# Performance work log

Hardware: AMD Instinct MI355X
Metric: run time of the kernel (lower is better)

Reference implementation:

```python
import jax, jax.numpy as jnp
import numpy as np

A, L, D_ATOM, D_PROT, B = 2048, 512, 128, 128, 64
H1, H2 = 512, 256


def setup_inputs() -> dict:
    key = jax.random.key(0)
    ks = jax.random.split(key, 10)
    atom_embed = jax.random.normal(ks[0], (A, D_ATOM), dtype=jnp.float32)
    protSeq_embed = jax.random.normal(ks[1], (B, L, D_PROT), dtype=jnp.float32)
    atom_splits = jnp.sort(jax.random.randint(ks[2], (A,), 0, B))
    # attention bilinear weight (atom_dim, prot_dim); scaled so exp(score) stays finite
    W_att = jax.random.normal(ks[3], (D_ATOM, D_PROT), dtype=jnp.float32) / np.float32(D_ATOM)
    cdim = D_ATOM + D_PROT
    W1 = jax.random.normal(ks[4], (cdim, H1), dtype=jnp.float32) / np.sqrt(np.float32(cdim))
    b1 = jnp.zeros((H1,), dtype=jnp.float32)
    W2 = jax.random.normal(ks[5], (H1, H2), dtype=jnp.float32) / np.sqrt(np.float32(H1))
    b2 = jnp.zeros((H2,), dtype=jnp.float32)
    Wo = jax.random.normal(ks[6], (H2, 1), dtype=jnp.float32) / np.sqrt(np.float32(H2))
    bo = jnp.zeros((1,), dtype=jnp.float32)
    return {"atom_embed": atom_embed, "protSeq_embed": protSeq_embed,
            "atom_splits": atom_splits, "W_att": W_att,
            "W1": W1, "b1": b1, "W2": W2, "b2": b2, "Wo": Wo, "bo": bo}


def reference(atom_embed, protSeq_embed, atom_splits, W_att, W1, b1, W2, b2, Wo, bo):
    batch = protSeq_embed.shape[0]
    # bilinear attention scores: S[a, l] = atom[a] @ W_att @ prot[seg[a], l]
    X = atom_embed @ W_att                              # [A, D_PROT]
    prot_g = protSeq_embed[atom_splits]                 # [A, L, D_PROT] (gather)
    S = jnp.einsum('ad,ald->al', X, prot_g)             # [A, L]
    # segment softmax over atoms within each molecule (on max-over-protein score)
    Wc = jnp.exp(jnp.max(S, axis=-1, keepdims=True))    # [A, 1]
    Sc = jax.ops.segment_sum(Wc, atom_splits, num_segments=batch)[atom_splits]
    aa = Wc / Sc                                        # [A, 1]
    atom_pool = jax.ops.segment_sum(aa * atom_embed, atom_splits, num_segments=batch)  # [B, D_ATOM]
    # protein attention: segment-max pooled scores -> softmax over residues
    Wp = jax.ops.segment_max(S, atom_splits, num_segments=batch)  # [B, L]
    ap = jax.nn.softmax(Wp, axis=-1)
    prot_pool = jnp.einsum('bl,bld->bd', ap, protSeq_embed)       # [B, D_PROT]
    h = jnp.concatenate([atom_pool, prot_pool], axis=-1)
    h = jax.nn.relu(h @ W1 + b1)
    h = jax.nn.relu(h @ W2 + b2)
    return h @ Wo + bo                                  # [B, 1]
```

## Files before the change

kernel.cpp:

```cpp
#include <hip/hip_runtime.h>
#include <math.h>

#define A_N 2048
#define L_N 512
#define D 128
#define B_N 64
#define H1_N 512
#define H2_N 256
#define NCHUNK 16
#define CL 32

typedef __attribute__((ext_vector_type(8))) short short8;
typedef __attribute__((ext_vector_type(4))) float f32x4;

__device__ __forceinline__ int lb_dev(const int* __restrict__ arr, int n, int val) {
    int lo = 0, hi = n;
    while (lo < hi) { int mid = (lo + hi) >> 1; if (arr[mid] < val) lo = mid + 1; else hi = mid; }
    return lo;
}

__device__ __forceinline__ float blk_sum(float v, float* red, int tid) {
    #pragma unroll
    for (int off = 32; off >= 1; off >>= 1) v += __shfl_xor(v, off);
    __syncthreads();
    if ((tid & 63) == 0) red[tid >> 6] = v;
    __syncthreads();
    return red[0] + red[1] + red[2] + red[3];
}

__device__ __forceinline__ unsigned short f2bf(float f) {
    unsigned int u = __float_as_uint(f);
    return (unsigned short)((u + 0x7FFFu + ((u >> 16) & 1u)) >> 16);
}
__device__ __forceinline__ float bf2f(unsigned short h) {
    return __uint_as_float(((unsigned int)h) << 16);
}

__global__ __launch_bounds__(256) void k1_xmul(const float* __restrict__ atom_embed,
                                               const float* __restrict__ W_att,
                                               const float* __restrict__ bo,
                                               const int* __restrict__ splits,
                                               unsigned short* __restrict__ Xh,
                                               unsigned short* __restrict__ Xl,
                                               float* __restrict__ out,
                                               int* __restrict__ segoff) {
    __shared__ float ae[8][128];
    const int tid = threadIdx.x;
    const int bid = blockIdx.x;
    if (bid == 0) {
        if (tid < B_N) out[tid] = bo[0];
        if (tid <= B_N) segoff[tid] = lb_dev(splits, A_N, tid);
    }
    const int a0 = bid * 8;
    float4 v = reinterpret_cast<const float4*>(atom_embed + (size_t)a0 * D)[tid];
    const int fi = tid * 4;
    *reinterpret_cast<float4*>(&ae[fi >> 7][fi & 127]) = v;
    __syncthreads();
    const int d = tid & 127;
    const int ai = tid >> 7;
    float acc0 = 0.f, acc1 = 0.f, acc2 = 0.f, acc3 = 0.f;
    #pragma unroll 16
    for (int k = 0; k < D; ++k) {
        const float w = W_att[k * D + d];
        acc0 += ae[ai + 0][k] * w;
        acc1 += ae[ai + 2][k] * w;
        acc2 += ae[ai + 4][k] * w;
        acc3 += ae[ai + 6][k] * w;
    }
    float accs[4] = {acc0, acc1, acc2, acc3};
    #pragma unroll
    for (int t = 0; t < 4; ++t) {
        const size_t idx = (size_t)(a0 + ai + 2 * t) * D + d;
        const unsigned short h = f2bf(accs[t]);
        Xh[idx] = h;
        Xl[idx] = f2bf(accs[t] - bf2f(h));
    }
}

__global__ __launch_bounds__(256, 3) void k2_scores(const unsigned short* __restrict__ Xh,
                                                    const unsigned short* __restrict__ Xl,
                                                    const float* __restrict__ prot,
                                                    const int* __restrict__ segoff,
                                                    float* __restrict__ rowmaxp,
                                                    float* __restrict__ ppart,
                                                    float* __restrict__ eWpart) {
    __shared__ float rm_part[2][128];
    __shared__ float cm_part[2][32];
    __shared__ float ews_s[CL];
    __shared__ float4 pred[8][32];

    const int tid = threadIdx.x;
    const int bid = blockIdx.x;
    const int b = bid & (B_N - 1);
    const int chunk = bid >> 6;
    const int l0 = chunk * CL;

    const int lane = tid & 63;
    const int w = tid >> 6;
    const int col = lane & 15;
    const int kb = lane >> 4;
    const int lt = w & 1;
    const int pair = w >> 1;

    short8 Bh[4], Bl[4];
    {
        const float4* pb = (const float4*)(prot + ((size_t)(b * L_N + l0 + lt * 16 + col)) * D);
        #pragma unroll
        for (int ks = 0; ks < 4; ++ks) {
            const float4 v0 = pb[ks * 8 + kb * 2];
            const float4 v1 = pb[ks * 8 + kb * 2 + 1];
            const float vv[8] = {v0.x, v0.y, v0.z, v0.w, v1.x, v1.y, v1.z, v1.w};
            short8 bh, bl;
            #pragma unroll
            for (int j = 0; j < 8; ++j) {
                const unsigned short h = f2bf(vv[j]);
                bh[j] = (short)h;
                bl[j] = (short)f2bf(vv[j] - bf2f(h));
            }
            Bh[ks] = bh; Bl[ks] = bl;
        }
    }
    const int s = segoff[b];
    const int n = segoff[b + 1] - s;

    ((float*)rm_part)[tid] = -INFINITY;
    if (tid < 64) ((float*)cm_part)[tid] = -INFINITY;
    __syncthreads();

    float cmrun = -INFINITY;
    for (int at = pair; at * 16 < n; at += 2) {
        const int arow = min(s + at * 16 + col, A_N - 1);
        const unsigned short* xh = Xh + (size_t)arow * D;
        const unsigned short* xl = Xl + (size_t)arow * D;
        short8 Ah[4], Al[4];
        #pragma unroll
        for (int ks = 0; ks < 4; ++ks) {
            Ah[ks] = *(const short8*)(xh + ks * 32 + kb * 8);
            Al[ks] = *(const short8*)(xl + ks * 32 + kb * 8);
        }
        f32x4 aHH = {0.f, 0.f, 0.f, 0.f};
        f32x4 aHL = {0.f, 0.f, 0.f, 0.f};
        f32x4 aLH = {0.f, 0.f, 0.f, 0.f};
        #pragma unroll
        for (int ks = 0; ks < 4; ++ks) {
            aHH = __builtin_amdgcn_mfma_f32_16x16x32_bf16(Ah[ks], Bh[ks], aHH, 0, 0, 0);
            aHL = __builtin_amdgcn_mfma_f32_16x16x32_bf16(Ah[ks], Bl[ks], aHL, 0, 0, 0);
            aLH = __builtin_amdgcn_mfma_f32_16x16x32_bf16(Al[ks], Bh[ks], aLH, 0, 0, 0);
        }
        float r[4];
        #pragma unroll
        for (int i = 0; i < 4; ++i) r[i] = aHH[i] + aHL[i] + aLH[i];

        float r0 = r[0], r1 = r[1], r2 = r[2], r3 = r[3];
        #pragma unroll
        for (int off = 1; off <= 8; off <<= 1) {
            r0 = fmaxf(r0, __shfl_xor(r0, off));
            r1 = fmaxf(r1, __shfl_xor(r1, off));
            r2 = fmaxf(r2, __shfl_xor(r2, off));
            r3 = fmaxf(r3, __shfl_xor(r3, off));
        }
        if (col == 0) {
            rm_part[lt][at * 16 + kb * 4 + 0] = r0;
            rm_part[lt][at * 16 + kb * 4 + 1] = r1;
            rm_part[lt][at * 16 + kb * 4 + 2] = r2;
            rm_part[lt][at * 16 + kb * 4 + 3] = r3;
        }
        const int rb = at * 16 + kb * 4;
        float cm = -INFINITY;
        if (rb + 0 < n) cm = fmaxf(cm, r[0]);
        if (rb + 1 < n) cm = fmaxf(cm, r[1]);
        if (rb + 2 < n) cm = fmaxf(cm, r[2]);
        if (rb + 3 < n) cm = fmaxf(cm, r[3]);
        cm = fmaxf(cm, __shfl_xor(cm, 16));
        cm = fmaxf(cm, __shfl_xor(cm, 32));
        cmrun = fmaxf(cmrun, cm);
    }
    if (kb == 0) cm_part[pair][lt * 16 + col] = cmrun;
    __syncthreads();

    if (tid < 128 && tid < n)
        rowmaxp[(size_t)(s + tid) * NCHUNK + chunk] = fmaxf(rm_part[0][tid], rm_part[1][tid]);
    if (tid >= 128 && tid < 128 + CL) {
        const int l = tid - 128;
        ews_s[l] = expf(fmaxf(cm_part[0][l], cm_part[1][l]));
    }
    __syncthreads();

    if (tid < 32) {
        float v = ews_s[tid];
        #pragma unroll
        for (int off = 1; off <= 16; off <<= 1) v += __shfl_xor(v, off);
        if (tid == 0) eWpart[b * NCHUNK + chunk] = v;
    }

    const int rg = tid >> 5, c4 = tid & 31;
    float4 pp4 = {0.f, 0.f, 0.f, 0.f};
    const float4* src = (const float4*)(prot + ((size_t)b * L_N + l0) * D);
    #pragma unroll
    for (int q = 0; q < 4; ++q) {
        const int i = tid + q * 256;
        const float4 v = src[i];
        const float wgt = ews_s[i >> 5];
        pp4.x += wgt * v.x; pp4.y += wgt * v.y;
        pp4.z += wgt * v.z; pp4.w += wgt * v.w;
    }
    pred[rg][c4] = pp4;
    __syncthreads();
    if (tid < 32) {
        float4 acc = pred[0][tid];
        #pragma unroll
        for (int gg = 1; gg < 8; ++gg) {
            const float4 t = pred[gg][tid];
            acc.x += t.x; acc.y += t.y; acc.z += t.z; acc.w += t.w;
        }
        float* dst = ppart + (size_t)(b * NCHUNK + chunk) * D + tid * 4;
        dst[0] = acc.x; dst[1] = acc.y; dst[2] = acc.z; dst[3] = acc.w;
    }
}

__global__ __launch_bounds__(256) void k3_pool(const float* __restrict__ atom_embed,
                                               const int* __restrict__ segoff,
                                               const float* __restrict__ rowmaxp,
                                               const float* __restrict__ ppart,
                                               const float* __restrict__ eWpart,
                                               float* __restrict__ HcT) {
    __shared__ float red[4];
    __shared__ float coef[512];
    __shared__ float4 pred[8][32];
    const int tid = threadIdx.x;
    const int b = blockIdx.x;
    const int s = segoff[b];
    const int n = segoff[b + 1] - s;

    float local = 0.f;
    for (int j = tid; j < n; j += 256) {
        const float* rp = rowmaxp + (size_t)(s + j) * NCHUNK;
        float m = rp[0];
        #pragma unroll
        for (int c = 1; c < NCHUNK; ++c) m = fmaxf(m, rp[c]);
        local += expf(m);
    }
    const float Sc = blk_sum(local, red, tid);

    const int d4 = tid & 31;
    const int ag = tid >> 5;
    const float4* ae4 = reinterpret_cast<const float4*>(atom_embed);
    float4 pool = {0.f, 0.f, 0.f, 0.f};
    for (int t0 = 0; t0 < n; t0 += 512) {
        const int cnt = min(512, n - t0);
        __syncthreads();
        for (int j = tid; j < cnt; j += 256) {
            const float* rp = rowmaxp + (size_t)(s + t0 + j) * NCHUNK;
            float m = rp[0];
            #pragma unroll
            for (int c = 1; c < NCHUNK; ++c) m = fmaxf(m, rp[c]);
            coef[j] = expf(m) / Sc;
        }
        __syncthreads();
        #pragma unroll 4
        for (int j = ag; j < cnt; j += 8) {
            const float c = coef[j];
            const float4 v = ae4[(size_t)(s + t0 + j) * (D / 4) + d4];
            pool.x += c * v.x; pool.y += c * v.y; pool.z += c * v.z; pool.w += c * v.w;
        }
    }
    __syncthreads();
    pred[ag][d4] = pool;
    __syncthreads();
    if (ag == 0) {
        float4 acc = pred[0][d4];
        #pragma unroll
        for (int gg = 1; gg < 8; ++gg) {
            const float4 t = pred[gg][d4];
            acc.x += t.x; acc.y += t.y; acc.z += t.z; acc.w += t.w;
        }
        HcT[(size_t)(d4 * 4 + 0) * B_N + b] = acc.x;
        HcT[(size_t)(d4 * 4 + 1) * B_N + b] = acc.y;
        HcT[(size_t)(d4 * 4 + 2) * B_N + b] = acc.z;
        HcT[(size_t)(d4 * 4 + 3) * B_N + b] = acc.w;
    }
    if (tid < 128) {
        float v = 0.f, ez = 0.f;
        #pragma unroll
        for (int c = 0; c < NCHUNK; ++c) {
            v  += ppart[(size_t)(b * NCHUNK + c) * D + tid];
            ez += eWpart[b * NCHUNK + c];
        }
        HcT[(size_t)(D + tid) * B_N + b] = v / ez;
    }
}

__global__ __launch_bounds__(256) void k4_h1(const float* __restrict__ HcT,
                                             const float* __restrict__ W1,
                                             const float* __restrict__ b1,
                                             float* __restrict__ H1T) {
    __shared__ float hr[4][64];
    const int tid = threadIdx.x;
    const int m = tid & 63;
    const int jh = (tid >> 6) & 1;
    const int kh = tid >> 7;
    const int j = blockIdx.x * 2 + jh;
    float acc = 0.f;
    const int k0 = kh * 128;
    #pragma unroll 8
    for (int k = k0; k < k0 + 128; ++k)
        acc += HcT[(size_t)k * B_N + m] * W1[(size_t)k * H1_N + j];
    hr[jh * 2 + kh][m] = acc;
    __syncthreads();
    if (kh == 0)
        H1T[(size_t)j * B_N + m] = fmaxf(hr[jh * 2][m] + hr[jh * 2 + 1][m] + b1[j], 0.f);
}

__global__ __launch_bounds__(256) void k5_h2(const float* __restrict__ H1T,
                                             const float* __restrict__ W2,
                                             const float* __restrict__ b2,
                                             const float* __restrict__ Wo,
                                             float* __restrict__ out) {
    __shared__ float hr[4][64];
    const int tid = threadIdx.x;
    const int m = tid & 63;
    const int kq = tid >> 6;
    const int j = blockIdx.x;
    float acc = 0.f;
    const int k0 = kq * 128;
    #pragma unroll 8
    for (int k = k0; k < k0 + 128; ++k)
        acc += H1T[(size_t)k * B_N + m] * W2[(size_t)k * H2_N + j];
    hr[kq][m] = acc;
    __syncthreads();
    if (kq == 0) {
        const float h2 = fmaxf(hr[0][m] + hr[1][m] + hr[2][m] + hr[3][m] + b2[j], 0.f);
        atomicAdd(out + m, h2 * Wo[j]);
    }
}

extern "C" void kernel_launch(void* const* d_in, const int* in_sizes, int n_in,
                              void* d_out, int out_size, void* d_ws, size_t ws_size,
                              hipStream_t stream) {
    const float* atom_embed = (const float*)d_in[0];
    const float* prot       = (const float*)d_in[1];
    const int*   splits     = (const int*)d_in[2];
    const float* W_att      = (const float*)d_in[3];
    const float* W1         = (const float*)d_in[4];
    const float* b1         = (const float*)d_in[5];
    const float* W2         = (const float*)d_in[6];
    const float* b2         = (const float*)d_in[7];
    const float* Wo         = (const float*)d_in[8];
    const float* bo         = (const float*)d_in[9];
    float* out = (float*)d_out;

    unsigned short* Xh = (unsigned short*)d_ws;
    unsigned short* Xl = Xh + (size_t)A_N * D;
    float* fp      = (float*)(Xl + (size_t)A_N * D);
    float* rowmaxp = fp;  fp += (size_t)A_N * NCHUNK;
    float* ppart   = fp;  fp += (size_t)B_N * NCHUNK * D;
    float* eWpart  = fp;  fp += B_N * NCHUNK;
    float* HcT     = fp;  fp += 2 * D * B_N;
    float* H1T     = fp;  fp += H1_N * B_N;
    int*   segoff  = (int*)fp;

    hipLaunchKernelGGL(k1_xmul,  dim3(A_N / 8),        dim3(256), 0, stream,
                       atom_embed, W_att, bo, splits, Xh, Xl, out, segoff);
    hipLaunchKernelGGL(k2_scores, dim3(B_N * NCHUNK),  dim3(256), 0, stream,
                       Xh, Xl, prot, segoff, rowmaxp, ppart, eWpart);
    hipLaunchKernelGGL(k3_pool,  dim3(B_N),            dim3(256), 0, stream,
                       atom_embed, segoff, rowmaxp, ppart, eWpart, HcT);
    hipLaunchKernelGGL(k4_h1,    dim3(H1_N / 2),       dim3(256), 0, stream, HcT, W1, b1, H1T);
    hipLaunchKernelGGL(k5_h2,    dim3(H2_N),           dim3(256), 0, stream, H1T, W2, b2, Wo, out);
}
```

Baseline: 48.40 us.

## Fuse X projection and pooling into scores kernel with last-block reduction

Removes the separate X = atom@W_att kernel and the pooling kernel. Each score block now recomputes X for its molecule's atoms with split-bf16 MFMA into shared memory, then computes scores. The last-arriving chunk block per molecule, found through an atomic counter, does the segment pooling. This cuts two launches and the Xh/Xl round trip through global memory, at the cost of computing X 16 times per atom, reloading and converting W_att in every atom tile, and adding a serial tail in the last block.

```diff
diff --git a/kernel.cpp b/kernel.cpp
--- a/kernel.cpp
+++ b/kernel.cpp
@@ -9,6 +9,7 @@
 #define H2_N 256
 #define NCHUNK 16
 #define CL 32
+#define PST 136
 
 typedef __attribute__((ext_vector_type(8))) short short8;
 typedef __attribute__((ext_vector_type(4))) float f32x4;
@@ -36,58 +37,33 @@
     return __uint_as_float(((unsigned int)h) << 16);
 }
 
-__global__ __launch_bounds__(256) void k1_xmul(const float* __restrict__ atom_embed,
-                                               const float* __restrict__ W_att,
+__global__ __launch_bounds__(256) void k0_init(const int* __restrict__ splits,
                                                const float* __restrict__ bo,
-                                               const int* __restrict__ splits,
-                                               unsigned short* __restrict__ Xh,
-                                               unsigned short* __restrict__ Xl,
-                                               float* __restrict__ out,
-                                               int* __restrict__ segoff) {
-    __shared__ float ae[8][128];
+                                               int* __restrict__ segoff,
+                                               int* __restrict__ cnt,
+                                               float* __restrict__ out) {
     const int tid = threadIdx.x;
-    const int bid = blockIdx.x;
-    if (bid == 0) {
-        if (tid < B_N) out[tid] = bo[0];
-        if (tid <= B_N) segoff[tid] = lb_dev(splits, A_N, tid);
-    }
-    const int a0 = bid * 8;
-    float4 v = reinterpret_cast<const float4*>(atom_embed + (size_t)a0 * D)[tid];
-    const int fi = tid * 4;
-    *reinterpret_cast<float4*>(&ae[fi >> 7][fi & 127]) = v;
-    __syncthreads();
-    const int d = tid & 127;
-    const int ai = tid >> 7;
-    float acc0 = 0.f, acc1 = 0.f, acc2 = 0.f, acc3 = 0.f;
-    #pragma unroll 16
-    for (int k = 0; k < D; ++k) {
-        const float w = W_att[k * D + d];
-        acc0 += ae[ai + 0][k] * w;
-        acc1 += ae[ai + 2][k] * w;
-        acc2 += ae[ai + 4][k] * w;
-        acc3 += ae[ai + 6][k] * w;
-    }
-    float accs[4] = {acc0, acc1, acc2, acc3};
-    #pragma unroll
-    for (int t = 0; t < 4; ++t) {
-        const size_t idx = (size_t)(a0 + ai + 2 * t) * D + d;
-        const unsigned short h = f2bf(accs[t]);
-        Xh[idx] = h;
-        Xl[idx] = f2bf(accs[t] - bf2f(h));
-    }
-}
-
-__global__ __launch_bounds__(256, 3) void k2_scores(const unsigned short* __restrict__ Xh,
-                                                    const unsigned short* __restrict__ Xl,
-                                                    const float* __restrict__ prot,
-                                                    const int* __restrict__ segoff,
-                                                    float* __restrict__ rowmaxp,
-                                                    float* __restrict__ ppart,
-                                                    float* __restrict__ eWpart) {
-    __shared__ float rm_part[2][128];
+    if (tid <= B_N) segoff[tid] = lb_dev(splits, A_N, tid);
+    if (tid < B_N) { cnt[tid] = 0; out[tid] = bo[0]; }
+}
+
+__global__ __launch_bounds__(256, 2) void k2_fused(const float* __restrict__ atom_embed,
+                                                   const float* __restrict__ prot,
+                                                   const float* __restrict__ W_att,
+                                                   const int* __restrict__ segoff,
+                                                   float* __restrict__ rowmaxp,
+                                                   float* __restrict__ ppart,
+                                                   float* __restrict__ eWpart,
+                                                   float* __restrict__ HcT,
+                                                   int* __restrict__ cnt) {
+    __shared__ unsigned short Xs_h[32 * PST], Xs_l[32 * PST];
+    __shared__ float rm_part[2][32];
     __shared__ float cm_part[2][32];
     __shared__ float ews_s[CL];
     __shared__ float4 pred[8][32];
+    __shared__ float coef[256];
+    __shared__ float red[4];
+    __shared__ int isLast;
 
     const int tid = threadIdx.x;
     const int bid = blockIdx.x;
@@ -102,7 +78,7 @@
     const int lt = w & 1;
     const int pair = w >> 1;
 
-    short8 Bh[4], Bl[4];
+    short8 PBh[4], PBl[4];
     {
         const float4* pb = (const float4*)(prot + ((size_t)(b * L_N + l0 + lt * 16 + col)) * D);
         #pragma unroll
@@ -117,94 +93,153 @@
                 bh[j] = (short)h;
                 bl[j] = (short)f2bf(vv[j] - bf2f(h));
             }
-            Bh[ks] = bh; Bl[ks] = bl;
+            PBh[ks] = bh; PBl[ks] = bl;
         }
     }
     const int s = segoff[b];
     const int n = segoff[b + 1] - s;
 
-    ((float*)rm_part)[tid] = -INFINITY;
-    if (tid < 64) ((float*)cm_part)[tid] = -INFINITY;
-    __syncthreads();
-
     float cmrun = -INFINITY;
-    for (int at = pair; at * 16 < n; at += 2) {
-        const int arow = min(s + at * 16 + col, A_N - 1);
-        const unsigned short* xh = Xh + (size_t)arow * D;
-        const unsigned short* xl = Xl + (size_t)arow * D;
-        short8 Ah[4], Al[4];
-        #pragma unroll
-        for (int ks = 0; ks < 4; ++ks) {
-            Ah[ks] = *(const short8*)(xh + ks * 32 + kb * 8);
-            Al[ks] = *(const short8*)(xl + ks * 32 + kb * 8);
-        }
-        f32x4 aHH = {0.f, 0.f, 0.f, 0.f};
-        f32x4 aHL = {0.f, 0.f, 0.f, 0.f};
-        f32x4 aLH = {0.f, 0.f, 0.f, 0.f};
-        #pragma unroll
-        for (int ks = 0; ks < 4; ++ks) {
-            aHH = __builtin_amdgcn_mfma_f32_16x16x32_bf16(Ah[ks], Bh[ks], aHH, 0, 0, 0);
-            aHL = __builtin_amdgcn_mfma_f32_16x16x32_bf16(Ah[ks], Bl[ks], aHL, 0, 0, 0);
-            aLH = __builtin_amdgcn_mfma_f32_16x16x32_bf16(Al[ks], Bh[ks], aLH, 0, 0, 0);
-        }
-        float r[4];
-        #pragma unroll
-        for (int i = 0; i < 4; ++i) r[i] = aHH[i] + aHL[i] + aLH[i];
-
-        float r0 = r[0], r1 = r[1], r2 = r[2], r3 = r[3];
-        #pragma unroll
-        for (int off = 1; off <= 8; off <<= 1) {
-            r0 = fmaxf(r0, __shfl_xor(r0, off));
-            r1 = fmaxf(r1, __shfl_xor(r1, off));
-            r2 = fmaxf(r2, __shfl_xor(r2, off));
-            r3 = fmaxf(r3, __shfl_xor(r3, off));
-        }
-        if (col == 0) {
-            rm_part[lt][at * 16 + kb * 4 + 0] = r0;
-            rm_part[lt][at * 16 + kb * 4 + 1] = r1;
-            rm_part[lt][at * 16 + kb * 4 + 2] = r2;
-            rm_part[lt][at * 16 + kb * 4 + 3] = r3;
-        }
-        const int rb = at * 16 + kb * 4;
-        float cm = -INFINITY;
-        if (rb + 0 < n) cm = fmaxf(cm, r[0]);
-        if (rb + 1 < n) cm = fmaxf(cm, r[1]);
-        if (rb + 2 < n) cm = fmaxf(cm, r[2]);
-        if (rb + 3 < n) cm = fmaxf(cm, r[3]);
-        cm = fmaxf(cm, __shfl_xor(cm, 16));
-        cm = fmaxf(cm, __shfl_xor(cm, 32));
-        cmrun = fmaxf(cmrun, cm);
-    }
+    for (int a0 = 0; a0 < n; a0 += 32) {
+        __syncthreads();
+
+        {
+            short8 WBh[2][4], WBl[2][4];
+            #pragma unroll
+            for (int ct = 0; ct < 2; ++ct) {
+                const int dcol = (w * 2 + ct) * 16 + col;
+                #pragma unroll
+                for (int ks = 0; ks < 4; ++ks) {
+                    short8 bh, bl;
+                    #pragma unroll
+                    for (int j = 0; j < 8; ++j) {
+                        const float wv = W_att[(size_t)(ks * 32 + kb * 8 + j) * D + dcol];
+                        const unsigned short h = f2bf(wv);
+                        bh[j] = (short)h;
+                        bl[j] = (short)f2bf(wv - bf2f(h));
+                    }
+                    WBh[ct][ks] = bh; WBl[ct][ks] = bl;
+                }
+            }
+            #pragma unroll
+            for (int m = 0; m < 2; ++m) {
+                const int ar = min(s + a0 + m * 16 + col, A_N - 1);
+                short8 Ah[4], Al[4];
+                #pragma unroll
+                for (int ks = 0; ks < 4; ++ks) {
+                    const float4* p = (const float4*)(atom_embed + (size_t)ar * D) + ks * 8 + kb * 2;
+                    const float4 v0 = p[0];
+                    const float4 v1 = p[1];
+                    const float vv[8] = {v0.x, v0.y, v0.z, v0.w, v1.x, v1.y, v1.z, v1.w};
+                    short8 ah, al;
+                    #pragma unroll
+                    for (int j = 0; j < 8; ++j) {
+                        const unsigned short h = f2bf(vv[j]);
+                        ah[j] = (short)h;
+                        al[j] = (short)f2bf(vv[j] - bf2f(h));
+                    }
+                    Ah[ks] = ah; Al[ks] = al;
+                }
+                #pragma unroll
+                for (int ct = 0; ct < 2; ++ct) {
+                    f32x4 aHH = {0.f, 0.f, 0.f, 0.f};
+                    f32x4 aHL = {0.f, 0.f, 0.f, 0.f};
+                    f32x4 aLH = {0.f, 0.f, 0.f, 0.f};
+                    #pragma unroll
+                    for (int ks = 0; ks < 4; ++ks) {
+                        aHH = __builtin_amdgcn_mfma_f32_16x16x32_bf16(Ah[ks], WBh[ct][ks], aHH, 0, 0, 0);
+                        aHL = __builtin_amdgcn_mfma_f32_16x16x32_bf16(Ah[ks], WBl[ct][ks], aHL, 0, 0, 0);
+                        aLH = __builtin_amdgcn_mfma_f32_16x16x32_bf16(Al[ks], WBh[ct][ks], aLH, 0, 0, 0);
+                    }
+                    const int dcol = (w * 2 + ct) * 16 + col;
+                    #pragma unroll
+                    for (int i = 0; i < 4; ++i) {
+                        const float xv = aHH[i] + aHL[i] + aLH[i];
+                        const int row = m * 16 + kb * 4 + i;
+                        const unsigned short h = f2bf(xv);
+                        Xs_h[row * PST + dcol] = h;
+                        Xs_l[row * PST + dcol] = f2bf(xv - bf2f(h));
+                    }
+                }
+            }
+        }
+        __syncthreads();
+
+        {
+            short8 Ah[4], Al[4];
+            const int xrow = pair * 16 + col;
+            #pragma unroll
+            for (int ks = 0; ks < 4; ++ks) {
+                Ah[ks] = *(const short8*)(Xs_h + xrow * PST + ks * 32 + kb * 8);
+                Al[ks] = *(const short8*)(Xs_l + xrow * PST + ks * 32 + kb * 8);
+            }
+            f32x4 aHH = {0.f, 0.f, 0.f, 0.f};
+            f32x4 aHL = {0.f, 0.f, 0.f, 0.f};
+            f32x4 aLH = {0.f, 0.f, 0.f, 0.f};
+            #pragma unroll
+            for (int ks = 0; ks < 4; ++ks) {
+                aHH = __builtin_amdgcn_mfma_f32_16x16x32_bf16(Ah[ks], PBh[ks], aHH, 0, 0, 0);
+                aHL = __builtin_amdgcn_mfma_f32_16x16x32_bf16(Ah[ks], PBl[ks], aHL, 0, 0, 0);
+                aLH = __builtin_amdgcn_mfma_f32_16x16x32_bf16(Al[ks], PBh[ks], aLH, 0, 0, 0);
+            }
+            float r[4];
+            #pragma unroll
+            for (int i = 0; i < 4; ++i) r[i] = aHH[i] + aHL[i] + aLH[i];
+
+            float r0 = r[0], r1 = r[1], r2 = r[2], r3 = r[3];
+            #pragma unroll
+            for (int off = 1; off <= 8; off <<= 1) {
+                r0 = fmaxf(r0, __shfl_xor(r0, off));
+                r1 = fmaxf(r1, __shfl_xor(r1, off));
+                r2 = fmaxf(r2, __shfl_xor(r2, off));
+                r3 = fmaxf(r3, __shfl_xor(r3, off));
+            }
+            if (col == 0) {
+                rm_part[lt][pair * 16 + kb * 4 + 0] = r0;
+                rm_part[lt][pair * 16 + kb * 4 + 1] = r1;
+                rm_part[lt][pair * 16 + kb * 4 + 2] = r2;
+                rm_part[lt][pair * 16 + kb * 4 + 3] = r3;
+            }
+            const int rb = a0 + pair * 16 + kb * 4;
+            float cm = -INFINITY;
+            if (rb + 0 < n) cm = fmaxf(cm, r[0]);
+            if (rb + 1 < n) cm = fmaxf(cm, r[1]);
+            if (rb + 2 < n) cm = fmaxf(cm, r[2]);
+            if (rb + 3 < n) cm = fmaxf(cm, r[3]);
+            cm = fmaxf(cm, __shfl_xor(cm, 16));
+            cm = fmaxf(cm, __shfl_xor(cm, 32));
+            cmrun = fmaxf(cmrun, cm);
+        }
+        __syncthreads();
+        if (tid < 32 && a0 + tid < n)
+            rowmaxp[(size_t)(s + a0 + tid) * NCHUNK + chunk] =
+                fmaxf(rm_part[0][tid], rm_part[1][tid]);
+    }
+
     if (kb == 0) cm_part[pair][lt * 16 + col] = cmrun;
     __syncthreads();
-
-    if (tid < 128 && tid < n)
-        rowmaxp[(size_t)(s + tid) * NCHUNK + chunk] = fmaxf(rm_part[0][tid], rm_part[1][tid]);
-    if (tid >= 128 && tid < 128 + CL) {
-        const int l = tid - 128;
-        ews_s[l] = expf(fmaxf(cm_part[0][l], cm_part[1][l]));
-    }
-    __syncthreads();
-
+    if (tid < CL) ews_s[tid] = expf(fmaxf(cm_part[0][tid], cm_part[1][tid]));
+    __syncthreads();
     if (tid < 32) {
         float v = ews_s[tid];
         #pragma unroll
         for (int off = 1; off <= 16; off <<= 1) v += __shfl_xor(v, off);
         if (tid == 0) eWpart[b * NCHUNK + chunk] = v;
     }
-
     const int rg = tid >> 5, c4 = tid & 31;
-    float4 pp4 = {0.f, 0.f, 0.f, 0.f};
-    const float4* src = (const float4*)(prot + ((size_t)b * L_N + l0) * D);
-    #pragma unroll
-    for (int q = 0; q < 4; ++q) {
-        const int i = tid + q * 256;
-        const float4 v = src[i];
-        const float wgt = ews_s[i >> 5];
-        pp4.x += wgt * v.x; pp4.y += wgt * v.y;
-        pp4.z += wgt * v.z; pp4.w += wgt * v.w;
-    }
-    pred[rg][c4] = pp4;
+    {
+        float4 pp4 = {0.f, 0.f, 0.f, 0.f};
+        const float4* src = (const float4*)(prot + ((size_t)b * L_N + l0) * D);
+        #pragma unroll
+        for (int q = 0; q < 4; ++q) {
+            const int i = tid + q * 256;
+            const float4 v = src[i];
+            const float wgt = ews_s[i >> 5];
+            pp4.x += wgt * v.x; pp4.y += wgt * v.y;
+            pp4.z += wgt * v.z; pp4.w += wgt * v.w;
+        }
+        pred[rg][c4] = pp4;
+    }
     __syncthreads();
     if (tid < 32) {
         float4 acc = pred[0][tid];
@@ -216,21 +251,17 @@
         float* dst = ppart + (size_t)(b * NCHUNK + chunk) * D + tid * 4;
         dst[0] = acc.x; dst[1] = acc.y; dst[2] = acc.z; dst[3] = acc.w;
     }
-}
-
-__global__ __launch_bounds__(256) void k3_pool(const float* __restrict__ atom_embed,
-                                               const int* __restrict__ segoff,
-                                               const float* __restrict__ rowmaxp,
-                                               const float* __restrict__ ppart,
-                                               const float* __restrict__ eWpart,
-                                               float* __restrict__ HcT) {
-    __shared__ float red[4];
-    __shared__ float coef[512];
-    __shared__ float4 pred[8][32];
-    const int tid = threadIdx.x;
-    const int b = blockIdx.x;
-    const int s = segoff[b];
-    const int n = segoff[b + 1] - s;
+    __syncthreads();
+
+    if (tid == 0) {
+        __threadfence();
+        int old = __hip_atomic_fetch_add(&cnt[b], 1, __ATOMIC_ACQ_REL, __HIP_MEMORY_SCOPE_AGENT);
+        isLast = (old == NCHUNK - 1) ? 1 : 0;
+    }
+    __syncthreads();
+    if (!isLast) return;
+    if (tid == 0) __threadfence();
+    __syncthreads();
 
     float local = 0.f;
     for (int j = tid; j < n; j += 256) {
@@ -242,14 +273,12 @@
     }
     const float Sc = blk_sum(local, red, tid);
 
-    const int d4 = tid & 31;
-    const int ag = tid >> 5;
-    const float4* ae4 = reinterpret_cast<const float4*>(atom_embed);
+    const float4* ae4 = (const float4*)atom_embed;
     float4 pool = {0.f, 0.f, 0.f, 0.f};
-    for (int t0 = 0; t0 < n; t0 += 512) {
-        const int cnt = min(512, n - t0);
-        __syncthreads();
-        for (int j = tid; j < cnt; j += 256) {
+    for (int t0 = 0; t0 < n; t0 += 256) {
+        const int cnt2 = min(256, n - t0);
+        __syncthreads();
+        for (int j = tid; j < cnt2; j += 256) {
             const float* rp = rowmaxp + (size_t)(s + t0 + j) * NCHUNK;
             float m = rp[0];
             #pragma unroll
@@ -257,27 +286,26 @@
             coef[j] = expf(m) / Sc;
         }
         __syncthreads();
-        #pragma unroll 4
-        for (int j = ag; j < cnt; j += 8) {
+        for (int j = rg; j < cnt2; j += 8) {
             const float c = coef[j];
-            const float4 v = ae4[(size_t)(s + t0 + j) * (D / 4) + d4];
+            const float4 v = ae4[(size_t)(s + t0 + j) * (D / 4) + c4];
             pool.x += c * v.x; pool.y += c * v.y; pool.z += c * v.z; pool.w += c * v.w;
         }
     }
     __syncthreads();
-    pred[ag][d4] = pool;
-    __syncthreads();
-    if (ag == 0) {
-        float4 acc = pred[0][d4];
+    pred[rg][c4] = pool;
+    __syncthreads();
+    if (rg == 0) {
+        float4 acc = pred[0][c4];
         #pragma unroll
         for (int gg = 1; gg < 8; ++gg) {
-            const float4 t = pred[gg][d4];
+            const float4 t = pred[gg][c4];
             acc.x += t.x; acc.y += t.y; acc.z += t.z; acc.w += t.w;
         }
-        HcT[(size_t)(d4 * 4 + 0) * B_N + b] = acc.x;
-        HcT[(size_t)(d4 * 4 + 1) * B_N + b] = acc.y;
-        HcT[(size_t)(d4 * 4 + 2) * B_N + b] = acc.z;
-        HcT[(size_t)(d4 * 4 + 3) * B_N + b] = acc.w;
+        HcT[(size_t)(c4 * 4 + 0) * B_N + b] = acc.x;
+        HcT[(size_t)(c4 * 4 + 1) * B_N + b] = acc.y;
+        HcT[(size_t)(c4 * 4 + 2) * B_N + b] = acc.z;
+        HcT[(size_t)(c4 * 4 + 3) * B_N + b] = acc.w;
     }
     if (tid < 128) {
         float v = 0.f, ez = 0.f;
@@ -349,22 +377,19 @@
     const float* bo         = (const float*)d_in[9];
     float* out = (float*)d_out;
 
-    unsigned short* Xh = (unsigned short*)d_ws;
-    unsigned short* Xl = Xh + (size_t)A_N * D;
-    float* fp      = (float*)(Xl + (size_t)A_N * D);
+    float* fp      = (float*)d_ws;
     float* rowmaxp = fp;  fp += (size_t)A_N * NCHUNK;
     float* ppart   = fp;  fp += (size_t)B_N * NCHUNK * D;
     float* eWpart  = fp;  fp += B_N * NCHUNK;
     float* HcT     = fp;  fp += 2 * D * B_N;
     float* H1T     = fp;  fp += H1_N * B_N;
-    int*   segoff  = (int*)fp;
-
-    hipLaunchKernelGGL(k1_xmul,  dim3(A_N / 8),        dim3(256), 0, stream,
-                       atom_embed, W_att, bo, splits, Xh, Xl, out, segoff);
-    hipLaunchKernelGGL(k2_scores, dim3(B_N * NCHUNK),  dim3(256), 0, stream,
-                       Xh, Xl, prot, segoff, rowmaxp, ppart, eWpart);
-    hipLaunchKernelGGL(k3_pool,  dim3(B_N),            dim3(256), 0, stream,
-                       atom_embed, segoff, rowmaxp, ppart, eWpart, HcT);
-    hipLaunchKernelGGL(k4_h1,    dim3(H1_N / 2),       dim3(256), 0, stream, HcT, W1, b1, H1T);
-    hipLaunchKernelGGL(k5_h2,    dim3(H2_N),           dim3(256), 0, stream, H1T, W2, b2, Wo, out);
-}
+    int*   segoff  = (int*)fp;  fp += 96;
+    int*   cnt     = (int*)fp;  fp += 64;
+
+    hipLaunchKernelGGL(k0_init,  dim3(1),             dim3(256), 0, stream,
+                       splits, bo, segoff, cnt, out);
+    hipLaunchKernelGGL(k2_fused, dim3(B_N * NCHUNK),  dim3(256), 0, stream,
+                       atom_embed, prot, W_att, segoff, rowmaxp, ppart, eWpart, HcT, cnt);
+    hipLaunchKernelGGL(k4_h1,    dim3(H1_N / 2),      dim3(256), 0, stream, HcT, W1, b1, H1T);
+    hipLaunchKernelGGL(k5_h2,    dim3(H2_N),          dim3(256), 0, stream, H1T, W2, b2, Wo, out);
+}
```

New measurement: 90.96 us. +87.9%, slower.

## Rework score and pooling kernels: per-wave 32-residue units, move protein pooling to k3

Applied to the files above, without the earlier changes.

k2 now gives each wave a 32-residue chunk and half the atom tiles, with two B tiles per wave. It writes row maxima straight to global memory and column maxima per half, so the shared-memory reductions and block syncs are gone. The protein-weighted pooling moves from k2 into k3, which now runs on 4x more blocks, each handling a 32-wide slice of the feature dimension. The aim is to shorten k2's critical path and spread k3's work across more CUs. In exchange, the k3 blocks recompute the exp/softmax normalisation redundantly and re-read the protein data.

```diff
diff --git a/kernel.cpp b/kernel.cpp
--- a/kernel.cpp
+++ b/kernel.cpp
@@ -8,7 +8,6 @@
 #define H1_N 512
 #define H2_N 256
 #define NCHUNK 16
-#define CL 32
 
 typedef __attribute__((ext_vector_type(8))) short short8;
 typedef __attribute__((ext_vector_type(4))) float f32x4;
@@ -48,8 +47,8 @@
     const int tid = threadIdx.x;
     const int bid = blockIdx.x;
     if (bid == 0) {
+        if (tid <= B_N) segoff[tid] = lb_dev(splits, A_N, tid);
         if (tid < B_N) out[tid] = bo[0];
-        if (tid <= B_N) segoff[tid] = lb_dev(splits, A_N, tid);
     }
     const int a0 = bid * 8;
     float4 v = reinterpret_cast<const float4*>(atom_embed + (size_t)a0 * D)[tid];
@@ -77,33 +76,26 @@
     }
 }
 
-__global__ __launch_bounds__(256, 3) void k2_scores(const unsigned short* __restrict__ Xh,
-                                                    const unsigned short* __restrict__ Xl,
-                                                    const float* __restrict__ prot,
-                                                    const int* __restrict__ segoff,
-                                                    float* __restrict__ rowmaxp,
-                                                    float* __restrict__ ppart,
-                                                    float* __restrict__ eWpart) {
-    __shared__ float rm_part[2][128];
-    __shared__ float cm_part[2][32];
-    __shared__ float ews_s[CL];
-    __shared__ float4 pred[8][32];
-
+__global__ __launch_bounds__(256) void k2_scores(const unsigned short* __restrict__ Xh,
+                                                 const unsigned short* __restrict__ Xl,
+                                                 const float* __restrict__ prot,
+                                                 const int* __restrict__ segoff,
+                                                 float* __restrict__ rowmaxp,
+                                                 float* __restrict__ cmaxp) {
     const int tid = threadIdx.x;
     const int bid = blockIdx.x;
     const int b = bid & (B_N - 1);
-    const int chunk = bid >> 6;
-    const int l0 = chunk * CL;
-
+    const int unit = (bid >> 6) * 4 + (tid >> 6);
+    const int chunk = unit & 15;
+    const int t0 = unit >> 4;
     const int lane = tid & 63;
-    const int w = tid >> 6;
     const int col = lane & 15;
     const int kb = lane >> 4;
-    const int lt = w & 1;
-    const int pair = w >> 1;
-
-    short8 Bh[4], Bl[4];
-    {
+    const int l0 = chunk * 32;
+
+    short8 Bh[2][4], Bl[2][4];
+    #pragma unroll
+    for (int lt = 0; lt < 2; ++lt) {
         const float4* pb = (const float4*)(prot + ((size_t)(b * L_N + l0 + lt * 16 + col)) * D);
         #pragma unroll
         for (int ks = 0; ks < 4; ++ks) {
@@ -117,19 +109,15 @@
                 bh[j] = (short)h;
                 bl[j] = (short)f2bf(vv[j] - bf2f(h));
             }
-            Bh[ks] = bh; Bl[ks] = bl;
+            Bh[lt][ks] = bh; Bl[lt][ks] = bl;
         }
     }
     const int s = segoff[b];
     const int n = segoff[b + 1] - s;
 
-    ((float*)rm_part)[tid] = -INFINITY;
-    if (tid < 64) ((float*)cm_part)[tid] = -INFINITY;
-    __syncthreads();
-
-    float cmrun = -INFINITY;
-    for (int at = pair; at * 16 < n; at += 2) {
-        const int arow = min(s + at * 16 + col, A_N - 1);
+    float cm0 = -INFINITY, cm1 = -INFINITY;
+    for (int t = t0; t * 16 < n; t += 2) {
+        const int arow = min(s + t * 16 + col, A_N - 1);
         const unsigned short* xh = Xh + (size_t)arow * D;
         const unsigned short* xl = Xl + (size_t)arow * D;
         short8 Ah[4], Al[4];
@@ -138,97 +126,74 @@
             Ah[ks] = *(const short8*)(xh + ks * 32 + kb * 8);
             Al[ks] = *(const short8*)(xl + ks * 32 + kb * 8);
         }
-        f32x4 aHH = {0.f, 0.f, 0.f, 0.f};
-        f32x4 aHL = {0.f, 0.f, 0.f, 0.f};
-        f32x4 aLH = {0.f, 0.f, 0.f, 0.f};
+        f32x4 a0HH = {0.f,0.f,0.f,0.f}, a0HL = {0.f,0.f,0.f,0.f}, a0LH = {0.f,0.f,0.f,0.f};
+        f32x4 a1HH = {0.f,0.f,0.f,0.f}, a1HL = {0.f,0.f,0.f,0.f}, a1LH = {0.f,0.f,0.f,0.f};
         #pragma unroll
         for (int ks = 0; ks < 4; ++ks) {
-            aHH = __builtin_amdgcn_mfma_f32_16x16x32_bf16(Ah[ks], Bh[ks], aHH, 0, 0, 0);
-            aHL = __builtin_amdgcn_mfma_f32_16x16x32_bf16(Ah[ks], Bl[ks], aHL, 0, 0, 0);
-            aLH = __builtin_amdgcn_mfma_f32_16x16x32_bf16(Al[ks], Bh[ks], aLH, 0, 0, 0);
-        }
-        float r[4];
-        #pragma unroll
-        for (int i = 0; i < 4; ++i) r[i] = aHH[i] + aHL[i] + aLH[i];
-
-        float r0 = r[0], r1 = r[1], r2 = r[2], r3 = r[3];
+            a0HH = __builtin_amdgcn_mfma_f32_16x16x32_bf16(Ah[ks], Bh[0][ks], a0HH, 0, 0, 0);
+            a0HL = __builtin_amdgcn_mfma_f32_16x16x32_bf16(Ah[ks], Bl[0][ks], a0HL, 0, 0, 0);
+            a0LH = __builtin_amdgcn_mfma_f32_16x16x32_bf16(Al[ks], Bh[0][ks], a0LH, 0, 0, 0);
+            a1HH = __builtin_amdgcn_mfma_f32_16x16x32_bf16(Ah[ks], Bh[1][ks], a1HH, 0, 0, 0);
+            a1HL = __builtin_amdgcn_mfma_f32_16x16x32_bf16(Ah[ks], Bl[1][ks], a1HL, 0, 0, 0);
+            a1LH = __builtin_amdgcn_mfma_f32_16x16x32_bf16(Al[ks], Bh[1][ks], a1LH, 0, 0, 0);
+        }
+        float ra[4], rb[4];
+        #pragma unroll
+        for (int i = 0; i < 4; ++i) {
+            ra[i] = a0HH[i] + a0HL[i] + a0LH[i];
+            rb[i] = a1HH[i] + a1HL[i] + a1LH[i];
+        }
+        float m0 = fmaxf(ra[0], rb[0]), m1 = fmaxf(ra[1], rb[1]);
+        float m2 = fmaxf(ra[2], rb[2]), m3 = fmaxf(ra[3], rb[3]);
         #pragma unroll
         for (int off = 1; off <= 8; off <<= 1) {
-            r0 = fmaxf(r0, __shfl_xor(r0, off));
-            r1 = fmaxf(r1, __shfl_xor(r1, off));
-            r2 = fmaxf(r2, __shfl_xor(r2, off));
-            r3 = fmaxf(r3, __shfl_xor(r3, off));
+            m0 = fmaxf(m0, __shfl_xor(m0, off));
+            m1 = fmaxf(m1, __shfl_xor(m1, off));
+            m2 = fmaxf(m2, __shfl_xor(m2, off));
+            m3 = fmaxf(m3, __shfl_xor(m3, off));
         }
         if (col == 0) {
-            rm_part[lt][at * 16 + kb * 4 + 0] = r0;
-            rm_part[lt][at * 16 + kb * 4 + 1] = r1;
-            rm_part[lt][at * 16 + kb * 4 + 2] = r2;
-            rm_part[lt][at * 16 + kb * 4 + 3] = r3;
-        }
-        const int rb = at * 16 + kb * 4;
-        float cm = -INFINITY;
-        if (rb + 0 < n) cm = fmaxf(cm, r[0]);
-        if (rb + 1 < n) cm = fmaxf(cm, r[1]);
-        if (rb + 2 < n) cm = fmaxf(cm, r[2]);
-        if (rb + 3 < n) cm = fmaxf(cm, r[3]);
-        cm = fmaxf(cm, __shfl_xor(cm, 16));
-        cm = fmaxf(cm, __shfl_xor(cm, 32));
-        cmrun = fmaxf(cmrun, cm);
-    }
-    if (kb == 0) cm_part[pair][lt * 16 + col] = cmrun;
-    __syncthreads();
-
-    if (tid < 128 && tid < n)
-        rowmaxp[(size_t)(s + tid) * NCHUNK + chunk] = fmaxf(rm_part[0][tid], rm_part[1][tid]);
-    if (tid >= 128 && tid < 128 + CL) {
-        const int l = tid - 128;
-        ews_s[l] = expf(fmaxf(cm_part[0][l], cm_part[1][l]));
-    }
-    __syncthreads();
-
-    if (tid < 32) {
-        float v = ews_s[tid];
-        #pragma unroll
-        for (int off = 1; off <= 16; off <<= 1) v += __shfl_xor(v, off);
-        if (tid == 0) eWpart[b * NCHUNK + chunk] = v;
-    }
-
-    const int rg = tid >> 5, c4 = tid & 31;
-    float4 pp4 = {0.f, 0.f, 0.f, 0.f};
-    const float4* src = (const float4*)(prot + ((size_t)b * L_N + l0) * D);
-    #pragma unroll
-    for (int q = 0; q < 4; ++q) {
-        const int i = tid + q * 256;
-        const float4 v = src[i];
-        const float wgt = ews_s[i >> 5];
-        pp4.x += wgt * v.x; pp4.y += wgt * v.y;
-        pp4.z += wgt * v.z; pp4.w += wgt * v.w;
-    }
-    pred[rg][c4] = pp4;
-    __syncthreads();
-    if (tid < 32) {
-        float4 acc = pred[0][tid];
-        #pragma unroll
-        for (int gg = 1; gg < 8; ++gg) {
-            const float4 t = pred[gg][tid];
-            acc.x += t.x; acc.y += t.y; acc.z += t.z; acc.w += t.w;
-        }
-        float* dst = ppart + (size_t)(b * NCHUNK + chunk) * D + tid * 4;
-        dst[0] = acc.x; dst[1] = acc.y; dst[2] = acc.z; dst[3] = acc.w;
+            const int rbase = t * 16 + kb * 4;
+            float mm[4] = {m0, m1, m2, m3};
+            #pragma unroll
+            for (int i = 0; i < 4; ++i)
+                if (rbase + i < n)
+                    rowmaxp[(size_t)(s + rbase + i) * NCHUNK + chunk] = mm[i];
+        }
+        const int rbase = t * 16 + kb * 4;
+        float c0 = -INFINITY, c1 = -INFINITY;
+        #pragma unroll
+        for (int i = 0; i < 4; ++i) {
+            if (rbase + i < n) {
+                c0 = fmaxf(c0, ra[i]);
+                c1 = fmaxf(c1, rb[i]);
+            }
+        }
+        c0 = fmaxf(c0, __shfl_xor(c0, 16)); c0 = fmaxf(c0, __shfl_xor(c0, 32));
+        c1 = fmaxf(c1, __shfl_xor(c1, 16)); c1 = fmaxf(c1, __shfl_xor(c1, 32));
+        cm0 = fmaxf(cm0, c0);
+        cm1 = fmaxf(cm1, c1);
+    }
+    if (kb == 0) {
+        cmaxp[(size_t)(b * 2 + t0) * L_N + l0 + col]      = cm0;
+        cmaxp[(size_t)(b * 2 + t0) * L_N + l0 + 16 + col] = cm1;
     }
 }
 
 __global__ __launch_bounds__(256) void k3_pool(const float* __restrict__ atom_embed,
+                                               const float* __restrict__ prot,
                                                const int* __restrict__ segoff,
                                                const float* __restrict__ rowmaxp,
-                                               const float* __restrict__ ppart,
-                                               const float* __restrict__ eWpart,
+                                               const float* __restrict__ cmaxp,
                                                float* __restrict__ HcT) {
     __shared__ float red[4];
     __shared__ float coef[512];
-    __shared__ float4 pred[8][32];
-    const int tid = threadIdx.x;
-    const int b = blockIdx.x;
+    __shared__ float ews_s[L_N];
+    __shared__ float4 pred[32][8];
+    const int tid = threadIdx.x;
+    const int bid = blockIdx.x;
+    const int b = bid & (B_N - 1);
+    const int dq = bid >> 6;
     const int s = segoff[b];
     const int n = segoff[b + 1] - s;
 
@@ -242,51 +207,101 @@
     }
     const float Sc = blk_sum(local, red, tid);
 
-    const int d4 = tid & 31;
-    const int ag = tid >> 5;
-    const float4* ae4 = reinterpret_cast<const float4*>(atom_embed);
+    float lz = 0.f;
+    for (int l = tid; l < L_N; l += 256) {
+        const float m = fmaxf(cmaxp[(size_t)(b * 2) * L_N + l],
+                              cmaxp[(size_t)(b * 2 + 1) * L_N + l]);
+        const float e = expf(m);
+        ews_s[l] = e;
+        lz += e;
+    }
+    const float Z = blk_sum(lz, red, tid);
+
+    const int d8 = tid & 7;
+    const int rg = tid >> 3;
+
+    const float4* ae4 = (const float4*)atom_embed;
     float4 pool = {0.f, 0.f, 0.f, 0.f};
-    for (int t0 = 0; t0 < n; t0 += 512) {
-        const int cnt = min(512, n - t0);
+    for (int base = 0; base < n; base += 512) {
+        const int cnt = min(512, n - base);
         __syncthreads();
         for (int j = tid; j < cnt; j += 256) {
-            const float* rp = rowmaxp + (size_t)(s + t0 + j) * NCHUNK;
+            const float* rp = rowmaxp + (size_t)(s + base + j) * NCHUNK;
             float m = rp[0];
             #pragma unroll
             for (int c = 1; c < NCHUNK; ++c) m = fmaxf(m, rp[c]);
             coef[j] = expf(m) / Sc;
         }
         __syncthreads();
-        #pragma unroll 4
-        for (int j = ag; j < cnt; j += 8) {
+        #pragma unroll 2
+        for (int j = rg; j < cnt; j += 32) {
             const float c = coef[j];
-            const float4 v = ae4[(size_t)(s + t0 + j) * (D / 4) + d4];
+            const float4 v = ae4[(size_t)(s + base + j) * (D / 4) + dq * 8 + d8];
             pool.x += c * v.x; pool.y += c * v.y; pool.z += c * v.z; pool.w += c * v.w;
         }
     }
-    __syncthreads();
-    pred[ag][d4] = pool;
-    __syncthreads();
-    if (ag == 0) {
-        float4 acc = pred[0][d4];
-        #pragma unroll
-        for (int gg = 1; gg < 8; ++gg) {
-            const float4 t = pred[gg][d4];
-            acc.x += t.x; acc.y += t.y; acc.z += t.z; acc.w += t.w;
-        }
-        HcT[(size_t)(d4 * 4 + 0) * B_N + b] = acc.x;
-        HcT[(size_t)(d4 * 4 + 1) * B_N + b] = acc.y;
-        HcT[(size_t)(d4 * 4 + 2) * B_N + b] = acc.z;
-        HcT[(size_t)(d4 * 4 + 3) * B_N + b] = acc.w;
-    }
-    if (tid < 128) {
-        float v = 0.f, ez = 0.f;
-        #pragma unroll
-        for (int c = 0; c < NCHUNK; ++c) {
-            v  += ppart[(size_t)(b * NCHUNK + c) * D + tid];
-            ez += eWpart[b * NCHUNK + c];
-        }
-        HcT[(size_t)(D + tid) * B_N + b] = v / ez;
+
+    const float4* pr4 = (const float4*)prot;
+    float4 pp = {0.f, 0.f, 0.f, 0.f};
+    #pragma unroll 4
+    for (int l = rg; l < L_N; l += 32) {
+        const float wgt = ews_s[l];
+        const float4 v = pr4[((size_t)b * L_N + l) * (D / 4) + dq * 8 + d8];
+        pp.x += wgt * v.x; pp.y += wgt * v.y; pp.z += wgt * v.z; pp.w += wgt * v.w;
+    }
+
+    __syncthreads();
+    pred[rg][d8] = pool;
+    __syncthreads();
+    if (rg < 8) {
+        float4 a = pred[rg][d8];
+        #pragma unroll
+        for (int k = 1; k < 4; ++k) {
+            const float4 t = pred[rg + 8 * k][d8];
+            a.x += t.x; a.y += t.y; a.z += t.z; a.w += t.w;
+        }
+        pred[rg][d8] = a;
+    }
+    __syncthreads();
+    if (tid < 8) {
+        float4 a = pred[0][tid];
+        #pragma unroll
+        for (int g = 1; g < 8; ++g) {
+            const float4 t = pred[g][tid];
+            a.x += t.x; a.y += t.y; a.z += t.z; a.w += t.w;
+        }
+        const int dbase = dq * 32 + tid * 4;
+        HcT[(size_t)(dbase + 0) * B_N + b] = a.x;
+        HcT[(size_t)(dbase + 1) * B_N + b] = a.y;
+        HcT[(size_t)(dbase + 2) * B_N + b] = a.z;
+        HcT[(size_t)(dbase + 3) * B_N + b] = a.w;
+    }
+    __syncthreads();
+    pred[rg][d8] = pp;
+    __syncthreads();
+    if (rg < 8) {
+        float4 a = pred[rg][d8];
+        #pragma unroll
+        for (int k = 1; k < 4; ++k) {
+            const float4 t = pred[rg + 8 * k][d8];
+            a.x += t.x; a.y += t.y; a.z += t.z; a.w += t.w;
+        }
+        pred[rg][d8] = a;
+    }
+    __syncthreads();
+    if (tid < 8) {
+        float4 a = pred[0][tid];
+        #pragma unroll
+        for (int g = 1; g < 8; ++g) {
+            const float4 t = pred[g][tid];
+            a.x += t.x; a.y += t.y; a.z += t.z; a.w += t.w;
+        }
+        const float invZ = 1.f / Z;
+        const int dbase = D + dq * 32 + tid * 4;
+        HcT[(size_t)(dbase + 0) * B_N + b] = a.x * invZ;
+        HcT[(size_t)(dbase + 1) * B_N + b] = a.y * invZ;
+        HcT[(size_t)(dbase + 2) * B_N + b] = a.z * invZ;
+        HcT[(size_t)(dbase + 3) * B_N + b] = a.w * invZ;
     }
 }
 
@@ -353,18 +368,17 @@
     unsigned short* Xl = Xh + (size_t)A_N * D;
     float* fp      = (float*)(Xl + (size_t)A_N * D);
     float* rowmaxp = fp;  fp += (size_t)A_N * NCHUNK;
-    float* ppart   = fp;  fp += (size_t)B_N * NCHUNK * D;
-    float* eWpart  = fp;  fp += B_N * NCHUNK;
+    float* cmaxp   = fp;  fp += (size_t)B_N * 2 * L_N;
     float* HcT     = fp;  fp += 2 * D * B_N;
     float* H1T     = fp;  fp += H1_N * B_N;
     int*   segoff  = (int*)fp;
 
-    hipLaunchKernelGGL(k1_xmul,  dim3(A_N / 8),        dim3(256), 0, stream,
+    hipLaunchKernelGGL(k1_xmul,  dim3(A_N / 8),   dim3(256), 0, stream,
                        atom_embed, W_att, bo, splits, Xh, Xl, out, segoff);
-    hipLaunchKernelGGL(k2_scores, dim3(B_N * NCHUNK),  dim3(256), 0, stream,
-                       Xh, Xl, prot, segoff, rowmaxp, ppart, eWpart);
-    hipLaunchKernelGGL(k3_pool,  dim3(B_N),            dim3(256), 0, stream,
-                       atom_embed, segoff, rowmaxp, ppart, eWpart, HcT);
-    hipLaunchKernelGGL(k4_h1,    dim3(H1_N / 2),       dim3(256), 0, stream, HcT, W1, b1, H1T);
-    hipLaunchKernelGGL(k5_h2,    dim3(H2_N),           dim3(256), 0, stream, H1T, W2, b2, Wo, out);
-}
+    hipLaunchKernelGGL(k2_scores, dim3(512),      dim3(256), 0, stream,
+                       Xh, Xl, prot, segoff, rowmaxp, cmaxp);
+    hipLaunchKernelGGL(k3_pool,  dim3(4 * B_N),   dim3(256), 0, stream,
+                       atom_embed, prot, segoff, rowmaxp, cmaxp, HcT);
+    hipLaunchKernelGGL(k4_h1,    dim3(H1_N / 2),  dim3(256), 0, stream, HcT, W1, b1, H1T);
+    hipLaunchKernelGGL(k5_h2,    dim3(H2_N),      dim3(256), 0, stream, H1T, W2, b2, Wo, out);
+}
```

Measured after the change: 47.11 us. 1.03x faster.
